# Kernel tuning notes

Hardware: AMD Instinct MI355X
Metric: run time of the kernel (lower is better)

## Reference

```python
import jax, jax.numpy as jnp
import numpy as np

SS, D, V = 64, 256, 10000
B, S = 16, 512


def setup_inputs() -> dict:
    key = jax.random.key(0)
    ks = jax.random.split(key, 7)
    scale = lambda fan_in: 1.0 / np.sqrt(fan_in)
    return {
        "x": jax.random.normal(ks[0], (B, S, D), dtype=jnp.float32),
        # nn.Linear(D, 4*ss): weight [4ss, D], bias [4ss]
        "Wxs_w": jax.random.uniform(ks[1], (4 * SS, D), jnp.float32, -scale(D), scale(D)),
        "Wxs_b": jax.random.uniform(ks[2], (4 * SS,), jnp.float32, -scale(D), scale(D)),
        # nn.Linear(ss, 4*ss)
        "Wss_w": jax.random.uniform(ks[3], (4 * SS, SS), jnp.float32, -scale(SS), scale(SS)),
        "Wss_b": jax.random.uniform(ks[4], (4 * SS,), jnp.float32, -scale(SS), scale(SS)),
        # nn.Linear(ss, V)
        "Wsy_w": jax.random.uniform(ks[5], (V, SS), jnp.float32, -scale(SS), scale(SS)),
        "Wsy_b": jax.random.uniform(ks[6], (V,), jnp.float32, -scale(SS), scale(SS)),
    }


def reference(x, Wxs_w, Wxs_b, Wss_w, Wss_b, Wsy_w, Wsy_b):
    b, s, _ = x.shape
    ss = Wss_w.shape[1]
    # Precompute input projections for all timesteps: [s, b, 4ss]
    xproj = jnp.einsum("bsd,kd->sbk", x, Wxs_w) + Wxs_b

    def step(carry, xp_t):
        h, c = carry
        comb = xp_t + h @ Wss_w.T + Wss_b  # [b, 4ss]
        f, i, g, o = jnp.split(comb, 4, axis=-1)
        f = jax.nn.sigmoid(f)
        i = jax.nn.sigmoid(i)
        o = jax.nn.sigmoid(o)
        g = jnp.tanh(g)
        c = c * f + i * g
        h = o * c  # NOTE: original code omits tanh(c) here; stay faithful
        return (h, c), h

    h0 = jnp.zeros((b, ss), dtype=x.dtype)
    c0 = jnp.zeros((b, ss), dtype=x.dtype)
    _, hs = jax.lax.scan(step, (h0, c0), xproj)  # hs: [s, b, ss]
    # Per-step vocab projection == batched projection of stacked hidden states
    y = jnp.einsum("sbh,vh->bsv", hs, Wsy_w) + Wsy_b  # [b, s, V]
    return y
```

## Files before the change

### kernel.cpp

```cpp
#include <hip/hip_runtime.h>

typedef unsigned short u16;
typedef unsigned int u32;

using short8 = __attribute__((ext_vector_type(8))) short;
using f32x4  = __attribute__((ext_vector_type(4))) float;
using f32x2  = __attribute__((ext_vector_type(2))) float;

#define SSEQ 512
#define BB   16
#define DD   256
#define G4   256
#define SSZ  64
#define VV   10000
#define VPAD 10112
#define MALL 8192

#define OFF_XHI   0u
#define OFF_XLO   4194304u
#define OFF_WHI   8388608u
#define OFF_WLO   8519680u
#define OFF_WSY   8650752u
#define OFF_XPROJ 9945088u
#define OFF_HS    18333696u

__device__ __forceinline__ u16 f2bf(float f) {
  u32 u = __float_as_uint(f);
  u32 r = (u + 0x7fffu + ((u >> 16) & 1u)) >> 16;
  return (u16)r;
}
__device__ __forceinline__ float bf2f(u16 h) {
  return __uint_as_float(((u32)h) << 16);
}
__device__ __forceinline__ f32x2 pkfma(f32x2 a, f32x2 b, f32x2 c) {
  asm("v_pk_fma_f32 %0, %1, %2, %0" : "+v"(c) : "v"(a), "v"(b));
  return c;
}
template <int CTRL>
__device__ __forceinline__ float qadd(float x) {
  int pv = __builtin_amdgcn_update_dpp(0, __float_as_int(x), CTRL, 0xf, 0xf, true);
  return x + __int_as_float(pv);
}
template <int CTRL>
__device__ __forceinline__ float qbcast(float x) {
  int pv = __builtin_amdgcn_update_dpp(0, __float_as_int(x), CTRL, 0xf, 0xf, true);
  return __int_as_float(pv);
}

#define NX 2097152
#define NW 65536
#define NP 647168
__global__ void k0_convert(const float* __restrict__ x, const float* __restrict__ Wxs,
                           const float* __restrict__ Wsy,
                           u16* __restrict__ xhi, u16* __restrict__ xlo,
                           u16* __restrict__ whi, u16* __restrict__ wlo,
                           u16* __restrict__ wsyb) {
  int i = blockIdx.x * 256 + threadIdx.x;
  if (i < NX) {
    float v = x[i]; u16 h = f2bf(v);
    xhi[i] = h; xlo[i] = f2bf(v - bf2f(h));
  } else if (i < NX + NW) {
    int j = i - NX;
    float v = Wxs[j]; u16 h = f2bf(v);
    whi[j] = h; wlo[j] = f2bf(v - bf2f(h));
  } else if (i < NX + NW + NP) {
    int j = i - NX - NW;
    wsyb[j] = (j < VV * SSZ) ? f2bf(Wsy[j]) : (u16)0;
  }
}

__global__ __launch_bounds__(256) void k1_xproj(
    const u16* __restrict__ xhi, const u16* __restrict__ xlo,
    const u16* __restrict__ whi, const u16* __restrict__ wlo,
    const float* __restrict__ bias, float* __restrict__ xproj) {
  int bid = blockIdx.x;
  int mb = bid >> 1, nb = bid & 1;
  int tid = threadIdx.x, l = tid & 63, wid = tid >> 6;
  int wm = wid >> 1, wv = wid & 1;
  int m0 = mb * 128 + wm * 64, n0 = nb * 128 + wv * 64;
  int lr = l & 15, lg = l >> 4;

  f32x4 acc[4][4];
#pragma unroll
  for (int a = 0; a < 4; a++)
#pragma unroll
    for (int bq = 0; bq < 4; bq++) acc[a][bq] = (f32x4){0.f, 0.f, 0.f, 0.f};

#pragma unroll
  for (int p = 0; p < 3; p++) {
    const u16* A = (p == 1) ? xlo : xhi;
    const u16* B = (p == 2) ? wlo : whi;
#pragma unroll
    for (int ks = 0; ks < 8; ks++) {
      short8 af[4], bf_[4];
#pragma unroll
      for (int fm = 0; fm < 4; fm++)
        af[fm] = *(const short8*)(A + (size_t)(m0 + fm * 16 + lr) * 256 + ks * 32 + lg * 8);
#pragma unroll
      for (int fv = 0; fv < 4; fv++)
        bf_[fv] = *(const short8*)(B + (size_t)(n0 + fv * 16 + lr) * 256 + ks * 32 + lg * 8);
#pragma unroll
      for (int fm = 0; fm < 4; fm++)
#pragma unroll
        for (int fv = 0; fv < 4; fv++)
          acc[fm][fv] = __builtin_amdgcn_mfma_f32_16x16x32_bf16(af[fm], bf_[fv], acc[fm][fv], 0, 0, 0);
    }
  }
#pragma unroll
  for (int fv = 0; fv < 4; fv++) {
    int j = n0 + fv * 16 + lr;
    float bj = bias[j];
#pragma unroll
    for (int fm = 0; fm < 4; fm++)
#pragma unroll
      for (int r = 0; r < 4; r++) {
        int m = m0 + fm * 16 + lg * 4 + r;
        xproj[(size_t)m * 256 + j] = acc[fm][fv][r] + bj;
      }
  }
}

__global__ __launch_bounds__(512, 1) __attribute__((amdgpu_waves_per_eu(2, 2)))
void k2_scan(
    const float* __restrict__ xproj, const float* __restrict__ Wss,
    const float* __restrict__ Wssb, u16* __restrict__ hsb) {
  __shared__ float hbuf[2][2][64];

  int tid = threadIdx.x;
  int w = tid >> 6, l = tid & 63;
  int bb = w >> 2, wv = w & 3;
  int b = blockIdx.x * 2 + bb;
  int oo = l >> 2, ks = l & 3;
  int jj = wv * 16 + oo;
  int ks16 = ks * 16;

  f32x2 wr[32];
#pragma unroll
  for (int g = 0; g < 4; g++) {
    const f32x2* pw = (const f32x2*)(Wss + (size_t)(g * 64 + jj) * 64 + ks16);
#pragma unroll
    for (int q = 0; q < 8; q++) wr[g * 8 + q] = pw[q];
  }
  float mybias = Wssb[ks * 64 + jj];

  float kk = (ks == 2) ? 2.885390082f : -1.442695041f;
  float Ac = (ks == 2) ? 1.f : 0.f;
  float Bc = (ks == 2) ? -2.f : 1.f;

  const float* xqp = xproj + (size_t)b * SSEQ * 256 + ks * 64 + jj;
  float xs0 = xqp[0 * 256];
  float xs1 = xqp[1 * 256];
  float xs2 = xqp[2 * 256];
  float xs3 = xqp[3 * 256];

  u16* hout = hsb + (size_t)b * SSEQ * 64 + jj;

  if (tid < 256) ((float*)hbuf)[tid] = 0.f;
  __syncthreads();

  float c = 0.f;

#define STEP(T, XS, RB, WB) { \
    f32x4 h4[4]; \
    const f32x4* hb = (const f32x4*)&hbuf[bb][RB][ks16]; \
    h4[0] = hb[0]; h4[1] = hb[1]; h4[2] = hb[2]; h4[3] = hb[3]; \
    float p[4]; \
    _Pragma("unroll") \
    for (int g = 0; g < 4; g++) { \
      f32x2 a0 = (f32x2){0.f, 0.f}, a1 = (f32x2){0.f, 0.f}; \
      _Pragma("unroll") \
      for (int q = 0; q < 4; q++) { \
        f32x2 hA = (f32x2){h4[q][0], h4[q][1]}; \
        f32x2 hB = (f32x2){h4[q][2], h4[q][3]}; \
        a0 = pkfma(hA, wr[g * 8 + 2 * q], a0); \
        a1 = pkfma(hB, wr[g * 8 + 2 * q + 1], a1); \
      } \
      f32x2 ps = a0 + a1; \
      p[g] = ps[0] + ps[1]; \
    } \
    _Pragma("unroll") \
    for (int g = 0; g < 4; g++) p[g] = qadd<0x4E>(qadd<0xB1>(p[g])); \
    float myp = (ks == 1) ? p[1] : p[0]; \
    myp = (ks == 2) ? p[2] : myp; \
    myp = (ks == 3) ? p[3] : myp; \
    float aa = myp + XS + mybias; \
    if ((T) + 4 < SSEQ) XS = xqp[(size_t)((T) + 4) * 256]; \
    float z = exp2f(kk * aa); \
    float act = fmaf(Bc, __builtin_amdgcn_rcpf(z + 1.f), Ac); \
    float fg = qbcast<0x00>(act); \
    float ig = qbcast<0x55>(act); \
    float gg = qbcast<0xAA>(act); \
    float og = qbcast<0xFF>(act); \
    c = fmaf(c, fg, ig * gg); \
    float hn = og * c;   \
    if (ks == 0) { \
      hbuf[bb][WB][jj] = hn; \
      __builtin_nontemporal_store(f2bf(hn), hout + (size_t)(T) * 64); \
    } \
    asm volatile("s_waitcnt lgkmcnt(0)\n\ts_barrier" ::: "memory"); \
  }

  for (int t = 0; t < SSEQ; t += 4) {
    STEP(t + 0, xs0, 1, 0)
    STEP(t + 1, xs1, 0, 1)
    STEP(t + 2, xs2, 1, 0)
    STEP(t + 3, xs3, 0, 1)
  }
#undef STEP
}

__global__ __launch_bounds__(256) void k3_y(
    const u16* __restrict__ hsb, const u16* __restrict__ wsyb,
    const float* __restrict__ bias, float* __restrict__ y) {
  __shared__ float ltile[128][132];
  int bid = blockIdx.x;
  int mb = bid / 79, vb = bid - mb * 79;
  int tid = threadIdx.x, l = tid & 63, wid = tid >> 6;
  int wm = wid >> 1, wv = wid & 1;
  int m0 = mb * 128 + wm * 64, v0 = vb * 128 + wv * 64;
  int lr = l & 15, lg = l >> 4;

  f32x4 acc[4][4];
#pragma unroll
  for (int a = 0; a < 4; a++)
#pragma unroll
    for (int bq = 0; bq < 4; bq++) acc[a][bq] = (f32x4){0.f, 0.f, 0.f, 0.f};

#pragma unroll
  for (int ks = 0; ks < 2; ks++) {
    short8 af[4], bf_[4];
#pragma unroll
    for (int fm = 0; fm < 4; fm++)
      af[fm] = *(const short8*)(hsb + (size_t)(m0 + fm * 16 + lr) * 64 + ks * 32 + lg * 8);
#pragma unroll
    for (int fv = 0; fv < 4; fv++)
      bf_[fv] = *(const short8*)(wsyb + (size_t)(v0 + fv * 16 + lr) * 64 + ks * 32 + lg * 8);
#pragma unroll
    for (int fv = 0; fv < 4; fv++)
#pragma unroll
      for (int fm = 0; fm < 4; fm++)
        acc[fv][fm] = __builtin_amdgcn_mfma_f32_16x16x32_bf16(bf_[fv], af[fm], acc[fv][fm], 0, 0, 0);
  }

#pragma unroll
  for (int fv = 0; fv < 4; fv++) {
    int vl = wv * 64 + fv * 16 + lg * 4;
    float bv0 = bias[v0 - wv * 64 + vl];
    bv0 = (vb * 128 + vl < VV) ? bias[vb * 128 + vl] : 0.f;
    float bv1 = (vb * 128 + vl + 1 < VV) ? bias[vb * 128 + vl + 1] : 0.f;
    float bv2 = (vb * 128 + vl + 2 < VV) ? bias[vb * 128 + vl + 2] : 0.f;
    float bv3 = (vb * 128 + vl + 3 < VV) ? bias[vb * 128 + vl + 3] : 0.f;
#pragma unroll
    for (int fm = 0; fm < 4; fm++) {
      int ml = wm * 64 + fm * 16 + lr;
      ltile[ml][vl + 0] = acc[fv][fm][0] + bv0;
      ltile[ml][vl + 1] = acc[fv][fm][1] + bv1;
      ltile[ml][vl + 2] = acc[fv][fm][2] + bv2;
      ltile[ml][vl + 3] = acc[fv][fm][3] + bv3;
    }
  }
  __syncthreads();

  int rr0 = tid >> 5;
  int c4 = (tid & 31) * 4;
#pragma unroll
  for (int it = 0; it < 16; it++) {
    int ml = it * 8 + rr0;
    int m = mb * 128 + ml;
    int v = vb * 128 + c4;
    if (v + 3 < VV) {
      float4 o;
      o.x = ltile[ml][c4 + 0];
      o.y = ltile[ml][c4 + 1];
      o.z = ltile[ml][c4 + 2];
      o.w = ltile[ml][c4 + 3];
      *(float4*)(y + (size_t)m * (size_t)VV + v) = o;
    }
  }
}

extern "C" void kernel_launch(void* const* d_in, const int* in_sizes, int n_in,
                              void* d_out, int out_size, void* d_ws, size_t ws_size,
                              hipStream_t stream) {
  const float* x     = (const float*)d_in[0];
  const float* Wxs_w = (const float*)d_in[1];
  const float* Wxs_b = (const float*)d_in[2];
  const float* Wss_w = (const float*)d_in[3];
  const float* Wss_b = (const float*)d_in[4];
  const float* Wsy_w = (const float*)d_in[5];
  const float* Wsy_b = (const float*)d_in[6];
  float* y = (float*)d_out;
  char* ws = (char*)d_ws;

  u16*   xhi   = (u16*)(ws + OFF_XHI);
  u16*   xlo   = (u16*)(ws + OFF_XLO);
  u16*   whi   = (u16*)(ws + OFF_WHI);
  u16*   wlo   = (u16*)(ws + OFF_WLO);
  u16*   wsyb  = (u16*)(ws + OFF_WSY);
  float* xproj = (float*)(ws + OFF_XPROJ);
  u16*   hsb   = (u16*)(ws + OFF_HS);

  k0_convert<<<(NX + NW + NP) / 256, 256, 0, stream>>>(x, Wxs_w, Wsy_w, xhi, xlo, whi, wlo, wsyb);
  k1_xproj<<<128, 256, 0, stream>>>(xhi, xlo, whi, wlo, Wxs_b, xproj);
  k2_scan<<<8, 512, 0, stream>>>(xproj, Wss_w, Wss_b, hsb);
  k3_y<<<64 * 79, 256, 0, stream>>>(hsb, wsyb, Wsy_b, y);
}
```

Before: 343.2 us.

## Rewrite LSTM scan as single-wave per batch with fp16 dot2 recurrence

The recurrent scan now runs one 64-lane wave per batch element instead of four waves per element across two elements per block. Each lane computes all four gates for its hidden unit with packed fp16 dot2 against an fp16-packed Wss, which is prepared in the convert kernel. The per-step block barrier and DPP reductions are removed, and h is exchanged through LDS in fp16 with only a waitcnt between steps. This shortens the serial per-step latency chain, at the cost of fp16 precision in the recurrence and more per-lane work (128 dot2 per step).

```diff
diff --git a/kernel.cpp b/kernel.cpp
--- a/kernel.cpp
+++ b/kernel.cpp
@@ -5,7 +5,7 @@
 
 using short8 = __attribute__((ext_vector_type(8))) short;
 using f32x4  = __attribute__((ext_vector_type(4))) float;
-using f32x2  = __attribute__((ext_vector_type(2))) float;
+using h2     = __attribute__((ext_vector_type(2))) _Float16;
 
 #define SSEQ 512
 #define BB   16
@@ -23,6 +23,7 @@
 #define OFF_WSY   8650752u
 #define OFF_XPROJ 9945088u
 #define OFF_HS    18333696u
+#define OFF_WPK   19382272u
 
 __device__ __forceinline__ u16 f2bf(float f) {
   u32 u = __float_as_uint(f);
@@ -32,29 +33,16 @@
 __device__ __forceinline__ float bf2f(u16 h) {
   return __uint_as_float(((u32)h) << 16);
 }
-__device__ __forceinline__ f32x2 pkfma(f32x2 a, f32x2 b, f32x2 c) {
-  asm("v_pk_fma_f32 %0, %1, %2, %0" : "+v"(c) : "v"(a), "v"(b));
-  return c;
-}
-template <int CTRL>
-__device__ __forceinline__ float qadd(float x) {
-  int pv = __builtin_amdgcn_update_dpp(0, __float_as_int(x), CTRL, 0xf, 0xf, true);
-  return x + __int_as_float(pv);
-}
-template <int CTRL>
-__device__ __forceinline__ float qbcast(float x) {
-  int pv = __builtin_amdgcn_update_dpp(0, __float_as_int(x), CTRL, 0xf, 0xf, true);
-  return __int_as_float(pv);
-}
 
 #define NX 2097152
 #define NW 65536
 #define NP 647168
+#define NF 8192
 __global__ void k0_convert(const float* __restrict__ x, const float* __restrict__ Wxs,
-                           const float* __restrict__ Wsy,
+                           const float* __restrict__ Wsy, const float* __restrict__ Wss,
                            u16* __restrict__ xhi, u16* __restrict__ xlo,
                            u16* __restrict__ whi, u16* __restrict__ wlo,
-                           u16* __restrict__ wsyb) {
+                           u16* __restrict__ wsyb, u32* __restrict__ wpk) {
   int i = blockIdx.x * 256 + threadIdx.x;
   if (i < NX) {
     float v = x[i]; u16 h = f2bf(v);
@@ -66,6 +54,15 @@
   } else if (i < NX + NW + NP) {
     int j = i - NX - NW;
     wsyb[j] = (j < VV * SSZ) ? f2bf(Wsy[j]) : (u16)0;
+  } else if (i < NX + NW + NP + NF) {
+    int j = i - NX - NW - NP;
+    int g = j >> 11, rem = j & 2047;
+    int s = rem >> 5, kp = rem & 31;
+    int row = g * 64 + s;
+    h2 p;
+    p[0] = (_Float16)Wss[row * 64 + 2 * kp];
+    p[1] = (_Float16)Wss[row * 64 + 2 * kp + 1];
+    wpk[j] = *(u32*)&p;
   }
 }
 
@@ -120,91 +117,78 @@
   }
 }
 
-__global__ __launch_bounds__(512, 1) __attribute__((amdgpu_waves_per_eu(2, 2)))
-void k2_scan(
-    const float* __restrict__ xproj, const float* __restrict__ Wss,
+__global__ __launch_bounds__(64, 1) void k2_scan(
+    const float* __restrict__ xproj, const u32* __restrict__ wpk,
     const float* __restrict__ Wssb, u16* __restrict__ hsb) {
-  __shared__ float hbuf[2][2][64];
-
-  int tid = threadIdx.x;
-  int w = tid >> 6, l = tid & 63;
-  int bb = w >> 2, wv = w & 3;
-  int b = blockIdx.x * 2 + bb;
-  int oo = l >> 2, ks = l & 3;
-  int jj = wv * 16 + oo;
-  int ks16 = ks * 16;
-
-  f32x2 wr[32];
+  __shared__ u32 hsh[32];
+  int b = blockIdx.x, l = threadIdx.x;
+
+  h2 wp[4][32];
 #pragma unroll
   for (int g = 0; g < 4; g++) {
-    const f32x2* pw = (const f32x2*)(Wss + (size_t)(g * 64 + jj) * 64 + ks16);
-#pragma unroll
-    for (int q = 0; q < 8; q++) wr[g * 8 + q] = pw[q];
-  }
-  float mybias = Wssb[ks * 64 + jj];
-
-  float kk = (ks == 2) ? 2.885390082f : -1.442695041f;
-  float Ac = (ks == 2) ? 1.f : 0.f;
-  float Bc = (ks == 2) ? -2.f : 1.f;
-
-  const float* xqp = xproj + (size_t)b * SSEQ * 256 + ks * 64 + jj;
-  float xs0 = xqp[0 * 256];
-  float xs1 = xqp[1 * 256];
-  float xs2 = xqp[2 * 256];
-  float xs3 = xqp[3 * 256];
-
-  u16* hout = hsb + (size_t)b * SSEQ * 64 + jj;
-
-  if (tid < 256) ((float*)hbuf)[tid] = 0.f;
-  __syncthreads();
-
+    const u32* src = wpk + g * 2048 + l * 32;
+#pragma unroll
+    for (int kp = 0; kp < 32; kp++) {
+      u32 v = src[kp];
+      wp[g][kp] = *(h2*)&v;
+    }
+  }
+  float bias4[4];
+#pragma unroll
+  for (int g = 0; g < 4; g++) bias4[g] = Wssb[g * 64 + l];
+
+  const float* xpb = xproj + (size_t)b * SSEQ * 256 + l;
+  float xA[4], xB[4];
+#pragma unroll
+  for (int g = 0; g < 4; g++) { xA[g] = xpb[g * 64]; xB[g] = xpb[256 + g * 64]; }
+
+  if (l < 32) hsh[l] = 0;
+  asm volatile("s_waitcnt lgkmcnt(0)" ::: "memory");
+
+  u16* hout = hsb + (size_t)b * SSEQ * 64 + l;
   float c = 0.f;
 
-#define STEP(T, XS, RB, WB) { \
-    f32x4 h4[4]; \
-    const f32x4* hb = (const f32x4*)&hbuf[bb][RB][ks16]; \
-    h4[0] = hb[0]; h4[1] = hb[1]; h4[2] = hb[2]; h4[3] = hb[3]; \
-    float p[4]; \
+#define STEP(T, X) { \
+    u32 hw[32]; \
+    const uint4* hb4 = (const uint4*)hsh; \
     _Pragma("unroll") \
-    for (int g = 0; g < 4; g++) { \
-      f32x2 a0 = (f32x2){0.f, 0.f}, a1 = (f32x2){0.f, 0.f}; \
+    for (int q = 0; q < 8; q++) { \
+      uint4 r = hb4[q]; \
+      hw[4 * q + 0] = r.x; hw[4 * q + 1] = r.y; \
+      hw[4 * q + 2] = r.z; hw[4 * q + 3] = r.w; \
+    } \
+    float a0 = X[0] + bias4[0]; \
+    float a1 = X[1] + bias4[1]; \
+    float a2 = X[2] + bias4[2]; \
+    float a3 = X[3] + bias4[3]; \
+    _Pragma("unroll") \
+    for (int kp = 0; kp < 32; kp++) { \
+      h2 hh = *(h2*)&hw[kp]; \
+      a0 = __builtin_amdgcn_fdot2(hh, wp[0][kp], a0, false); \
+      a1 = __builtin_amdgcn_fdot2(hh, wp[1][kp], a1, false); \
+      a2 = __builtin_amdgcn_fdot2(hh, wp[2][kp], a2, false); \
+      a3 = __builtin_amdgcn_fdot2(hh, wp[3][kp], a3, false); \
+    } \
+    if ((T) + 2 < SSEQ) { \
+      const float* xn = xpb + (size_t)((T) + 2) * 256; \
       _Pragma("unroll") \
-      for (int q = 0; q < 4; q++) { \
-        f32x2 hA = (f32x2){h4[q][0], h4[q][1]}; \
-        f32x2 hB = (f32x2){h4[q][2], h4[q][3]}; \
-        a0 = pkfma(hA, wr[g * 8 + 2 * q], a0); \
-        a1 = pkfma(hB, wr[g * 8 + 2 * q + 1], a1); \
-      } \
-      f32x2 ps = a0 + a1; \
-      p[g] = ps[0] + ps[1]; \
+      for (int g = 0; g < 4; g++) X[g] = xn[g * 64]; \
     } \
-    _Pragma("unroll") \
-    for (int g = 0; g < 4; g++) p[g] = qadd<0x4E>(qadd<0xB1>(p[g])); \
-    float myp = (ks == 1) ? p[1] : p[0]; \
-    myp = (ks == 2) ? p[2] : myp; \
-    myp = (ks == 3) ? p[3] : myp; \
-    float aa = myp + XS + mybias; \
-    if ((T) + 4 < SSEQ) XS = xqp[(size_t)((T) + 4) * 256]; \
-    float z = exp2f(kk * aa); \
-    float act = fmaf(Bc, __builtin_amdgcn_rcpf(z + 1.f), Ac); \
-    float fg = qbcast<0x00>(act); \
-    float ig = qbcast<0x55>(act); \
-    float gg = qbcast<0xAA>(act); \
-    float og = qbcast<0xFF>(act); \
+    float fg = __builtin_amdgcn_rcpf(1.f + exp2f(-1.442695041f * a0)); \
+    float ig = __builtin_amdgcn_rcpf(1.f + exp2f(-1.442695041f * a1)); \
+    float gg = fmaf(-2.f, __builtin_amdgcn_rcpf(exp2f(2.885390082f * a2) + 1.f), 1.f); \
+    float og = __builtin_amdgcn_rcpf(1.f + exp2f(-1.442695041f * a3)); \
     c = fmaf(c, fg, ig * gg); \
-    float hn = og * c;   \
-    if (ks == 0) { \
-      hbuf[bb][WB][jj] = hn; \
-      __builtin_nontemporal_store(f2bf(hn), hout + (size_t)(T) * 64); \
-    } \
-    asm volatile("s_waitcnt lgkmcnt(0)\n\ts_barrier" ::: "memory"); \
-  }
-
-  for (int t = 0; t < SSEQ; t += 4) {
-    STEP(t + 0, xs0, 1, 0)
-    STEP(t + 1, xs1, 0, 1)
-    STEP(t + 2, xs2, 1, 0)
-    STEP(t + 3, xs3, 0, 1)
+    float hn = og * c;    \
+    _Float16 hf = (_Float16)hn; \
+    ((u16*)hsh)[l] = *(u16*)&hf; \
+    hout[(size_t)(T) * 64] = f2bf(hn);    \
+    asm volatile("s_waitcnt lgkmcnt(0)" ::: "memory"); \
+  }
+
+  for (int t = 0; t < SSEQ; t += 2) {
+    STEP(t, xA)
+    STEP(t + 1, xB)
   }
 #undef STEP
 }
@@ -245,8 +229,7 @@
 #pragma unroll
   for (int fv = 0; fv < 4; fv++) {
     int vl = wv * 64 + fv * 16 + lg * 4;
-    float bv0 = bias[v0 - wv * 64 + vl];
-    bv0 = (vb * 128 + vl < VV) ? bias[vb * 128 + vl] : 0.f;
+    float bv0 = (vb * 128 + vl     < VV) ? bias[vb * 128 + vl]     : 0.f;
     float bv1 = (vb * 128 + vl + 1 < VV) ? bias[vb * 128 + vl + 1] : 0.f;
     float bv2 = (vb * 128 + vl + 2 < VV) ? bias[vb * 128 + vl + 2] : 0.f;
     float bv3 = (vb * 128 + vl + 3 < VV) ? bias[vb * 128 + vl + 3] : 0.f;
@@ -299,9 +282,11 @@
   u16*   wsyb  = (u16*)(ws + OFF_WSY);
   float* xproj = (float*)(ws + OFF_XPROJ);
   u16*   hsb   = (u16*)(ws + OFF_HS);
-
-  k0_convert<<<(NX + NW + NP) / 256, 256, 0, stream>>>(x, Wxs_w, Wsy_w, xhi, xlo, whi, wlo, wsyb);
+  u32*   wpk   = (u32*)(ws + OFF_WPK);
+
+  k0_convert<<<(NX + NW + NP + NF) / 256, 256, 0, stream>>>(
+      x, Wxs_w, Wsy_w, Wss_w, xhi, xlo, whi, wlo, wsyb, wpk);
   k1_xproj<<<128, 256, 0, stream>>>(xhi, xlo, whi, wlo, Wxs_b, xproj);
-  k2_scan<<<8, 512, 0, stream>>>(xproj, Wss_w, Wss_b, hsb);
+  k2_scan<<<16, 64, 0, stream>>>(xproj, wpk, Wss_b, hsb);
   k3_y<<<64 * 79, 256, 0, stream>>>(hsb, wsyb, Wsy_b, y);
 }
```

Result: no change. 338.8 us (-1.3%).
